# Kernel optimization log

Measured on AMD Instinct MI355X. Metric: run time of the kernel, lower is better.

## Reference

```python
import jax, jax.numpy as jnp
import numpy as np

HEADS = 8
DIM_HEAD = 32
EPS = 1e-5


def _rel_index(h, w):
    # matches Attention._generate_relative_index (static, computed on host)
    coords = np.stack(np.meshgrid(np.arange(h), np.arange(w), indexing='ij')).reshape(2, -1)
    rel = coords[:, :, None] - coords[:, None, :]  # [2, n, n]
    rel[0] += h - 1
    rel[1] += w - 1
    rel[0] *= 2 * w - 1
    idx = rel.sum(0).reshape(-1)
    # torch.clamp(relative_index, 0, max_index) -- indices are already in range here
    return jnp.asarray(np.clip(idx, 0, (2 * h - 1) * (2 * w - 1) - 1))


def _layernorm(x, g, b):
    m = jnp.mean(x, axis=-1, keepdims=True)
    v = jnp.var(x, axis=-1, keepdims=True)
    return (x - m) * jax.lax.rsqrt(v + EPS) * g + b


def setup_inputs() -> dict:
    key = jax.random.key(0)
    ks = jax.random.split(key, 6)
    B, C, H, W = 64, 384, 16, 16
    inner = HEADS * DIM_HEAD  # 256
    hid = 4 * C               # 1536
    def nrm(k, shape, s=0.02):
        return jax.random.normal(k, shape, jnp.float32) * s
    return {
        'x': jax.random.normal(ks[0], (B, C, H, W), jnp.float32),
        'ln1_g': jnp.ones((C,), jnp.float32),
        'ln1_b': jnp.zeros((C,), jnp.float32),
        'w_qkv': nrm(ks[1], (C, 3 * inner)),
        'bias_table': nrm(ks[2], ((2 * H - 1) * (2 * W - 1), HEADS)),
        'w_out': nrm(ks[3], (inner, C)),
        'b_out': jnp.zeros((C,), jnp.float32),
        'ln2_g': jnp.ones((C,), jnp.float32),
        'ln2_b': jnp.zeros((C,), jnp.float32),
        'w_ff1': nrm(ks[4], (C, hid)),
        'b_ff1': jnp.zeros((hid,), jnp.float32),
        'w_ff2': nrm(ks[5], (hid, C)),
        'b_ff2': jnp.zeros((C,), jnp.float32),
    }


def reference(x, ln1_g, ln1_b, w_qkv, bias_table, w_out, b_out,
              ln2_g, ln2_b, w_ff1, b_ff1, w_ff2, b_ff2):
    B, C, H, W = x.shape
    n = H * W
    t = x.reshape(B, C, n).transpose(0, 2, 1)  # [B, n, C]

    # --- attention branch (PreNorm(LayerNorm) -> Attention) ---
    a = _layernorm(t, ln1_g, ln1_b)
    qkv = a @ w_qkv  # [B, n, 3*inner]
    q, k, v = jnp.split(qkv, 3, axis=-1)
    def split_heads(z):
        return z.reshape(B, n, HEADS, DIM_HEAD).transpose(0, 2, 1, 3)  # [B, h, n, d]
    q, k, v = split_heads(q), split_heads(k), split_heads(v)
    dots = jnp.einsum('bhid,bhjd->bhij', q, k) * (DIM_HEAD ** -0.5)
    idx = _rel_index(H, W)  # [n*n]
    rel_bias = bias_table[idx].reshape(n, n, HEADS).transpose(2, 0, 1)[None]  # [1, h, n, n]
    attn = jax.nn.softmax(dots + rel_bias, axis=-1)
    o = jnp.einsum('bhij,bhjd->bhid', attn, v)
    o = o.transpose(0, 2, 1, 3).reshape(B, n, HEADS * DIM_HEAD)
    attn_out = o @ w_out + b_out  # to_out Linear (dropout=0)

    # --- feedforward branch (PreNorm(LayerNorm) -> FFN) ---
    f = _layernorm(t, ln2_g, ln2_b)
    f = jax.nn.gelu(f @ w_ff1 + b_ff1, approximate=False) @ w_ff2 + b_ff2

    y = t + attn_out + f  # x_adjusted + attn_out + ff_out
    return y.transpose(0, 2, 1).reshape(B, C, H, W)
```

## Files before the change

kernel.cpp:

```cpp
#include <hip/hip_runtime.h>

typedef __bf16 bf16;
typedef __bf16 bf16x8 __attribute__((ext_vector_type(8)));
typedef float f32x4 __attribute__((ext_vector_type(4)));

__device__ __forceinline__ void gll16(const void* g, void* l) {
    __builtin_amdgcn_global_load_lds((const __attribute__((address_space(1))) void*)g,
                                     (__attribute__((address_space(3))) void*)l, 16, 0, 0);
}

__launch_bounds__(256)
__global__ void prep_kernel(const float* __restrict__ wqkv, const float* __restrict__ wout,
                            const float* __restrict__ wff1, const float* __restrict__ wff2,
                            bf16* __restrict__ wqkvT, bf16* __restrict__ woutT,
                            bf16* __restrict__ wff1T, bf16* __restrict__ wff2T,
                            const float* __restrict__ x,
                            const float* __restrict__ g1, const float* __restrict__ b1,
                            const float* __restrict__ g2, const float* __restrict__ b2,
                            bf16* __restrict__ a, bf16* __restrict__ f) {
    __shared__ __align__(16) float smem[12672 + 512 + 64];
    const int tid = threadIdx.x;
    int g = blockIdx.x;
    if (g < 1536) {
        float (*tl)[33] = (float (*)[33])smem;
        const float* in; bf16* out; int R, Cc, bx, by;
        if (g < 288)       { in = wqkv; out = wqkvT; R = 384;  Cc = 768;  bx = g % 24; by = g / 24; }
        else if (g < 384)  { g -= 288; in = wout; out = woutT; R = 256;  Cc = 384;  bx = g % 12; by = g / 12; }
        else if (g < 960)  { g -= 384; in = wff1; out = wff1T; R = 384;  Cc = 1536; bx = g % 48; by = g / 48; }
        else               { g -= 960; in = wff2; out = wff2T; R = 1536; Cc = 384;  bx = g % 12; by = g / 12; }
        const int c0 = bx * 32, r0 = by * 32;
        const int cl = tid & 31, r8 = tid >> 5;
#pragma unroll
        for (int k = 0; k < 4; k++) {
            int r = k * 8 + r8;
            tl[r][cl] = in[(size_t)(r0 + r) * Cc + c0 + cl];
        }
        __syncthreads();
#pragma unroll
        for (int k = 0; k < 4; k++) {
            int cc = k * 8 + r8;
            out[(size_t)(c0 + cc) * R + r0 + cl] = (bf16)tl[cl][cc];
        }
        return;
    }
    g -= 1536;
    float (*tile)[33] = (float (*)[33])smem;
    float (*S)[32]  = (float (*)[32])(smem + 12672);
    float (*SS)[32] = (float (*)[32])(smem + 12928);
    float* Mn = smem + 13184;
    float* Rs = smem + 13216;
    const int bb = g >> 3;
    const int i0 = (g & 7) * 32;
    {
        const int i_l = tid & 31, c_l = tid >> 5;
        const size_t base = (size_t)bb * 384 * 256 + i0 + i_l;
#pragma unroll 6
        for (int c = c_l; c < 384; c += 8)
            tile[c][i_l] = x[base + (size_t)c * 256];
    }
    __syncthreads();
    {
        const int i_s = tid & 31, p = tid >> 5;
        float s = 0.f, ss = 0.f;
#pragma unroll 6
        for (int j = 0; j < 48; j++) {
            float v = tile[p * 48 + j][i_s];
            s += v; ss += v * v;
        }
        S[p][i_s] = s; SS[p][i_s] = ss;
    }
    __syncthreads();
    if (tid < 32) {
        float t1 = 0.f, t2 = 0.f;
#pragma unroll
        for (int p = 0; p < 8; p++) { t1 += S[p][tid]; t2 += SS[p][tid]; }
        float mean = t1 * (1.0f / 384.0f);
        float var  = t2 * (1.0f / 384.0f) - mean * mean;
        Mn[tid] = mean;
        Rs[tid] = rsqrtf(var + 1e-5f);
    }
    __syncthreads();
    const int lane = tid & 63, w = tid >> 6;
#pragma unroll
    for (int rr = 0; rr < 8; rr++) {
        const int i = w * 8 + rr;
        const float mean = Mn[i], rstd = Rs[i];
        const size_t orow = ((size_t)bb * 256 + i0 + i) * 384;
#pragma unroll
        for (int pass = 0; pass < 6; pass++) {
            const int c = pass * 64 + lane;
            float nh = (tile[c][i] - mean) * rstd;
            a[orow + c] = (bf16)(nh * g1[c] + b1[c]);
            f[orow + c] = (bf16)(nh * g2[c] + b2[c]);
        }
    }
}

template <int EPI>
__launch_bounds__(256)
__global__ void gemm_bt(const bf16* __restrict__ A, const bf16* __restrict__ Bt,
                        const float* __restrict__ bias, bf16* __restrict__ C,
                        int M, int N, int K, int nx) {
    __shared__ bf16 lds[16384];
    bf16* lA = lds;
    bf16* lB = lds + 4096;
    const int tid = threadIdx.x;
    const int g = blockIdx.x;
    const int x = (g >> 3) % nx;
    const int y = (g & 7) + 8 * (g / (8 * nx));
    const int m0 = y * 128, n0 = x * 128;
    const int lane = tid & 63, w = tid >> 6;
    const int l16 = lane & 15, quad = lane >> 4;
    const int wm = (w & 1) * 64, wn = (w >> 1) * 64;

    f32x4 zero = {0.f, 0.f, 0.f, 0.f};
    f32x4 acc[4][4];
#pragma unroll
    for (int i = 0; i < 4; i++)
#pragma unroll
        for (int j = 0; j < 4; j++) acc[i][j] = zero;

    const int c0 = tid, c1 = tid + 256;
    const int r0 = c0 >> 2, k0c = (c0 & 3) * 8;
    const int r1 = c1 >> 2, k1c = (c1 & 3) * 8;
    const bf16* Abase = A + (size_t)m0 * K;
    const bf16* Bbase = Bt + (size_t)n0 * K;

    for (int kb = 0; kb < K; kb += 32) {
        gll16(Abase + (size_t)r0 * K + kb + k0c, lA + c0 * 8);
        gll16(Abase + (size_t)r1 * K + kb + k1c, lA + c1 * 8);
        gll16(Bbase + (size_t)r0 * K + kb + k0c, lB + c0 * 8);
        gll16(Bbase + (size_t)r1 * K + kb + k1c, lB + c1 * 8);
        __syncthreads();
        bf16x8 af[4], bfr[4];
#pragma unroll
        for (int i = 0; i < 4; i++)
            af[i] = *(const bf16x8*)(lA + (wm + i * 16 + l16) * 32 + quad * 8);
#pragma unroll
        for (int j = 0; j < 4; j++)
            bfr[j] = *(const bf16x8*)(lB + (wn + j * 16 + l16) * 32 + quad * 8);
#pragma unroll
        for (int i = 0; i < 4; i++)
#pragma unroll
            for (int j = 0; j < 4; j++)
                acc[i][j] = __builtin_amdgcn_mfma_f32_16x16x32_bf16(af[i], bfr[j], acc[i][j], 0, 0, 0);
        __syncthreads();
    }

#pragma unroll
    for (int j = 0; j < 4; j++) {
        const int col = wn + j * 16 + l16;
        float bv = 0.f;
        if (EPI >= 1) bv = bias[n0 + col];
#pragma unroll
        for (int i = 0; i < 4; i++) {
            const int row0 = wm + i * 16 + quad * 4;
#pragma unroll
            for (int r = 0; r < 4; r++) {
                float v = acc[i][j][r] + bv;
                if (EPI == 2) v = 0.5f * v * (1.0f + erff(v * 0.70710678118654752f));
                lds[(row0 + r) * 128 + col] = (bf16)v;
            }
        }
    }
    __syncthreads();
#pragma unroll
    for (int it = 0; it < 8; it++) {
        const int ch = tid + it * 256;
        const int row = ch >> 4, cc = (ch & 15) * 8;
        *(bf16x8*)(C + (size_t)(m0 + row) * N + n0 + cc) = *(const bf16x8*)(lds + row * 128 + cc);
    }
}

#define GEMM64_PROLOGUE_AND_KLOOP                                                   \
    const int tid = threadIdx.x;                                                    \
    const int g = blockIdx.x;                                                       \
    const int x_ = (g >> 3) % nx;                                                   \
    const int y_ = (g & 7) + 8 * (g / (8 * nx));                                    \
    const int m0 = y_ * 128, n0 = x_ * 64;                                          \
    const int lane = tid & 63, w = tid >> 6;                                        \
    const int l16 = lane & 15, quad = lane >> 4;                                    \
    const int wm = (w & 1) * 64, wn = (w >> 1) * 32;                                \
    f32x4 zero = {0.f, 0.f, 0.f, 0.f};                                              \
    f32x4 acc[4][2];                                                                \
    _Pragma("unroll") for (int i = 0; i < 4; i++)                                   \
        _Pragma("unroll") for (int j = 0; j < 2; j++) acc[i][j] = zero;             \
    const int c0 = tid, c1 = tid + 256;                                             \
    const int r0 = c0 >> 2, k0c = (c0 & 3) * 8;                                     \
    const int r1 = c1 >> 2, k1c = (c1 & 3) * 8;                                     \
    const bf16* Abase = A + (size_t)m0 * K;                                         \
    const bf16* Bbase = Bt + (size_t)n0 * K;                                        \
    for (int kb = 0; kb < K; kb += 32) {                                            \
        gll16(Abase + (size_t)r0 * K + kb + k0c, lA + c0 * 8);                      \
        gll16(Abase + (size_t)r1 * K + kb + k1c, lA + c1 * 8);                      \
        gll16(Bbase + (size_t)r0 * K + kb + k0c, lB + c0 * 8);                      \
        __syncthreads();                                                            \
        bf16x8 af[4], bfr[2];                                                       \
        _Pragma("unroll") for (int i = 0; i < 4; i++)                               \
            af[i] = *(const bf16x8*)(lA + (wm + i * 16 + l16) * 32 + quad * 8);     \
        _Pragma("unroll") for (int j = 0; j < 2; j++)                               \
            bfr[j] = *(const bf16x8*)(lB + (wn + j * 16 + l16) * 32 + quad * 8);    \
        _Pragma("unroll") for (int i = 0; i < 4; i++)                               \
            _Pragma("unroll") for (int j = 0; j < 2; j++)                           \
                acc[i][j] = __builtin_amdgcn_mfma_f32_16x16x32_bf16(af[i], bfr[j], acc[i][j], 0, 0, 0); \
        __syncthreads();                                                            \
    }

__launch_bounds__(256)
__global__ void gemm_bt_tr64(const bf16* __restrict__ A, const bf16* __restrict__ Bt,
                             const float* __restrict__ bias, bf16* __restrict__ Ct,
                             int M, int N, int K, int nx) {
    __shared__ bf16 lds[8448];
    bf16* lA = lds;
    bf16* lB = lds + 4096;
    GEMM64_PROLOGUE_AND_KLOOP
#pragma unroll
    for (int j = 0; j < 2; j++) {
        const int col = wn + j * 16 + l16;
        const float bv = bias[n0 + col];
#pragma unroll
        for (int i = 0; i < 4; i++) {
            const int row0 = wm + i * 16 + quad * 4;
#pragma unroll
            for (int r = 0; r < 4; r++)
                lds[col * 132 + row0 + r] = (bf16)(acc[i][j][r] + bv);
        }
    }
    __syncthreads();
    const int b = m0 >> 8, ib = m0 & 255;
#pragma unroll
    for (int it = 0; it < 4; it++) {
        const int ch = tid + it * 256;
        const int cl = ch >> 4, ic = (ch & 15) * 8;
        *(bf16x8*)(Ct + ((size_t)(b * 384 + n0 + cl) * 256 + ib + ic)) =
            *(const bf16x8*)(lds + cl * 132 + ic);
    }
}

__launch_bounds__(256)
__global__ void gemm_bt_final64(const bf16* __restrict__ A, const bf16* __restrict__ Bt,
                                const float* __restrict__ bias,
                                const float* __restrict__ xres, const bf16* __restrict__ attn_t,
                                float* __restrict__ out, int M, int N, int K, int nx) {
    __shared__ bf16 lds[8448];
    bf16* lA = lds;
    bf16* lB = lds + 4096;
    GEMM64_PROLOGUE_AND_KLOOP
#pragma unroll
    for (int j = 0; j < 2; j++) {
        const int col = wn + j * 16 + l16;
        const float bv = bias[n0 + col];
#pragma unroll
        for (int i = 0; i < 4; i++) {
            const int row0 = wm + i * 16 + quad * 4;
#pragma unroll
            for (int r = 0; r < 4; r++)
                lds[col * 132 + row0 + r] = (bf16)(acc[i][j][r] + bv);
        }
    }
    __syncthreads();
    const int b = m0 >> 8, ib = m0 & 255;
#pragma unroll
    for (int it = 0; it < 4; it++) {
        const int ch = tid + it * 256;
        const int cl = ch >> 4, ic = (ch & 15) * 8;
        const size_t base = (size_t)(b * 384 + n0 + cl) * 256 + ib + ic;
        bf16x8 ff = *(const bf16x8*)(lds + cl * 132 + ic);
        bf16x8 at = *(const bf16x8*)(attn_t + base);
#pragma unroll
        for (int e = 0; e < 8; e++)
            out[base + e] = xres[base + e] + (float)at[e] + (float)ff[e];
    }
}

__launch_bounds__(256)
__global__ void attn_kernel(const bf16* __restrict__ qkv,
                            const float* __restrict__ btab,
                            bf16* __restrict__ o) {
    __shared__ float sbias[961];
    __shared__ __align__(16) bf16 sVt[32][264];
    __shared__ __align__(16) bf16 sP[4][16][264];
    const int tid = threadIdx.x;
    const int qc = blockIdx.x & 3;
    const int h  = (blockIdx.x >> 2) & 7;
    const int bb = blockIdx.x >> 5;
    const int lane = tid & 63, w = tid >> 6;
    const int l16 = lane & 15, quad = lane >> 4;
    const size_t qkvb = (size_t)bb * 256 * 768;

    for (int e = tid; e < 961; e += 256) sbias[e] = btab[e * 8 + h];
#pragma unroll
    for (int it = 0; it < 32; it++) {
        int e = it * 256 + tid;
        int k = e >> 5, d = e & 31;
        sVt[d][k] = qkv[qkvb + (size_t)k * 768 + 512 + h * 32 + d];
    }
    __syncthreads();

    const int qbase = qc * 64 + w * 16;
    bf16x8 qf = *(const bf16x8*)(qkv + qkvb + (size_t)(qbase + l16) * 768 + h * 32 + quad * 8);
    f32x4 zero = {0.f, 0.f, 0.f, 0.f};
    f32x4 s[16];
#pragma unroll
    for (int kt = 0; kt < 16; kt++) {
        bf16x8 kf = *(const bf16x8*)(qkv + qkvb + (size_t)(kt * 16 + l16) * 768 + 256 + h * 32 + quad * 8);
        s[kt] = __builtin_amdgcn_mfma_f32_16x16x32_bf16(qf, kf, zero, 0, 0, 0);
    }
    const int qi0 = qbase + quad * 4;
    float mx[4] = {-1e30f, -1e30f, -1e30f, -1e30f};
#pragma unroll
    for (int kt = 0; kt < 16; kt++) {
        const int j = kt * 16 + l16;
        const int yj = j >> 4, xj = j & 15;
#pragma unroll
        for (int r = 0; r < 4; r++) {
            const int q = qi0 + r;
            const int tix = ((q >> 4) - yj + 15) * 31 + ((q & 15) - xj + 15);
            float v = s[kt][r] * 0.17677669529663687f + sbias[tix];
            s[kt][r] = v;
            mx[r] = fmaxf(mx[r], v);
        }
    }
#pragma unroll
    for (int r = 0; r < 4; r++)
        for (int msk = 1; msk < 16; msk <<= 1)
            mx[r] = fmaxf(mx[r], __shfl_xor(mx[r], msk, 64));
    float sum[4] = {0.f, 0.f, 0.f, 0.f};
#pragma unroll
    for (int kt = 0; kt < 16; kt++)
#pragma unroll
        for (int r = 0; r < 4; r++) {
            float e = __expf(s[kt][r] - mx[r]);
            s[kt][r] = e;
            sum[r] += e;
        }
#pragma unroll
    for (int r = 0; r < 4; r++) {
        for (int msk = 1; msk < 16; msk <<= 1)
            sum[r] += __shfl_xor(sum[r], msk, 64);
        sum[r] = 1.0f / sum[r];
    }
#pragma unroll
    for (int kt = 0; kt < 16; kt++)
#pragma unroll
        for (int r = 0; r < 4; r++)
            sP[w][quad * 4 + r][kt * 16 + l16] = (bf16)(s[kt][r] * sum[r]);
    f32x4 oacc[2];
    oacc[0] = zero; oacc[1] = zero;
#pragma unroll
    for (int ks = 0; ks < 8; ks++) {
        bf16x8 pf = *(const bf16x8*)(&sP[w][l16][ks * 32 + quad * 8]);
#pragma unroll
        for (int dt = 0; dt < 2; dt++) {
            bf16x8 vf = *(const bf16x8*)(&sVt[dt * 16 + l16][ks * 32 + quad * 8]);
            oacc[dt] = __builtin_amdgcn_mfma_f32_16x16x32_bf16(pf, vf, oacc[dt], 0, 0, 0);
        }
    }
#pragma unroll
    for (int dt = 0; dt < 2; dt++)
#pragma unroll
        for (int r = 0; r < 4; r++)
            o[(size_t)(bb * 256 + qbase + quad * 4 + r) * 256 + h * 32 + dt * 16 + l16] = (bf16)oacc[dt][r];
}

extern "C" void kernel_launch(void* const* d_in, const int* in_sizes, int n_in,
                              void* d_out, int out_size, void* d_ws, size_t ws_size,
                              hipStream_t stream) {
    const float* x    = (const float*)d_in[0];
    const float* g1   = (const float*)d_in[1];
    const float* b1   = (const float*)d_in[2];
    const float* wqkv = (const float*)d_in[3];
    const float* btab = (const float*)d_in[4];
    const float* wout = (const float*)d_in[5];
    const float* bout = (const float*)d_in[6];
    const float* g2   = (const float*)d_in[7];
    const float* b2   = (const float*)d_in[8];
    const float* wff1 = (const float*)d_in[9];
    const float* bff1 = (const float*)d_in[10];
    const float* wff2 = (const float*)d_in[11];
    const float* bff2 = (const float*)d_in[12];
    float* out = (float*)d_out;

    bf16* ws = (bf16*)d_ws;
    const size_t NA = 6291456;
    bf16* wqkvT = ws;
    bf16* woutT = wqkvT + 294912;
    bf16* wff1T = woutT + 98304;
    bf16* wff2T = wff1T + 589824;
    bf16* f_buf    = ws + 1572864;
    bf16* attn_t   = f_buf + NA;
    bf16* R        = attn_t + NA;
    bf16* a_buf    = R;
    bf16* qkv_buf  = R + NA;
    bf16* o_buf    = R;
    bf16* ffh_buf  = R;

    dim3 b256(256);
    prep_kernel<<<2048, b256, 0, stream>>>(wqkv, wout, wff1, wff2, wqkvT, woutT, wff1T, wff2T,
                                           x, g1, b1, g2, b2, a_buf, f_buf);

    gemm_bt<0><<<6 * 128, b256, 0, stream>>>(a_buf, wqkvT, nullptr, qkv_buf, 16384, 768, 384, 6);
    attn_kernel<<<2048, b256, 0, stream>>>(qkv_buf, btab, o_buf);
    gemm_bt_tr64<<<6 * 128, b256, 0, stream>>>(o_buf, woutT, bout, attn_t, 16384, 384, 256, 6);
    gemm_bt<2><<<12 * 128, b256, 0, stream>>>(f_buf, wff1T, bff1, ffh_buf, 16384, 1536, 384, 12);
    gemm_bt_final64<<<6 * 128, b256, 0, stream>>>(ffh_buf, wff2T, bff2, x, attn_t, out,
                                                  16384, 384, 1536, 6);
}
```

Measured before the change: 261.8 us.

## Reuse K/V across query chunks in attention and use fast GELU approximation

The attention kernel now processes all four query chunks per block, staging K into shared memory with async global-to-LDS loads and loading V with vectorized reads before transposing it. This removes the redundant per-chunk K/V reloads and scalar V gathers, at the cost of a 4x smaller grid and more serial work per block. Separately, the FF1 epilogue replaces exact erf GELU with an exp/reciprocal-based approximation, which cuts transcendental cost but slightly changes numerics.

```diff
diff --git a/kernel.cpp b/kernel.cpp
--- a/kernel.cpp
+++ b/kernel.cpp
@@ -7,6 +7,13 @@
 __device__ __forceinline__ void gll16(const void* g, void* l) {
     __builtin_amdgcn_global_load_lds((const __attribute__((address_space(1))) void*)g,
                                      (__attribute__((address_space(3))) void*)l, 16, 0, 0);
+}
+
+__device__ __forceinline__ float gelu_f(float v) {
+    float x2 = v * v;
+    float sn = v * fmaf(-0.0713540072f, x2, -1.5957691216f);
+    float e  = __expf(sn);
+    return v * __builtin_amdgcn_rcpf(1.0f + e);
 }
 
 __launch_bounds__(256)
@@ -158,7 +165,7 @@
 #pragma unroll
             for (int r = 0; r < 4; r++) {
                 float v = acc[i][j][r] + bv;
-                if (EPI == 2) v = 0.5f * v * (1.0f + erff(v * 0.70710678118654752f));
+                if (EPI == 2) v = gelu_f(v);
                 lds[(row0 + r) * 128 + col] = (bf16)v;
             }
         }
@@ -278,89 +285,104 @@
                             const float* __restrict__ btab,
                             bf16* __restrict__ o) {
     __shared__ float sbias[961];
+    __shared__ __align__(16) bf16 sK[256 * 32];
     __shared__ __align__(16) bf16 sVt[32][264];
     __shared__ __align__(16) bf16 sP[4][16][264];
     const int tid = threadIdx.x;
-    const int qc = blockIdx.x & 3;
-    const int h  = (blockIdx.x >> 2) & 7;
-    const int bb = blockIdx.x >> 5;
+    const int g = blockIdx.x;
+    const int h  = (g >> 3) & 7;
+    const int bb = (g & 7) + 8 * (g >> 6);
     const int lane = tid & 63, w = tid >> 6;
     const int l16 = lane & 15, quad = lane >> 4;
     const size_t qkvb = (size_t)bb * 256 * 768;
+    const bf16* Qbase = qkv + qkvb + h * 32;
+    const bf16* Kbase = qkv + qkvb + 256 + h * 32;
+    const bf16* Vbase = qkv + qkvb + 512 + h * 32;
 
     for (int e = tid; e < 961; e += 256) sbias[e] = btab[e * 8 + h];
 #pragma unroll
-    for (int it = 0; it < 32; it++) {
-        int e = it * 256 + tid;
-        int k = e >> 5, d = e & 31;
-        sVt[d][k] = qkv[qkvb + (size_t)k * 768 + 512 + h * 32 + d];
-    }
-    __syncthreads();
-
-    const int qbase = qc * 64 + w * 16;
-    bf16x8 qf = *(const bf16x8*)(qkv + qkvb + (size_t)(qbase + l16) * 768 + h * 32 + quad * 8);
+    for (int it = 0; it < 4; it++) {
+        const int ch = it * 256 + tid;
+        const int row = ch >> 2, d8 = (ch & 3) * 8;
+        gll16(Kbase + (size_t)row * 768 + d8, sK + ch * 8);
+    }
+#pragma unroll
+    for (int it = 0; it < 4; it++) {
+        const int ch = it * 256 + tid;
+        const int k = ch >> 2, d8 = (ch & 3) * 8;
+        bf16x8 vv = *(const bf16x8*)(Vbase + (size_t)k * 768 + d8);
+#pragma unroll
+        for (int j = 0; j < 8; j++)
+            sVt[d8 + j][k] = vv[j];
+    }
+    __syncthreads();
+
     f32x4 zero = {0.f, 0.f, 0.f, 0.f};
-    f32x4 s[16];
-#pragma unroll
-    for (int kt = 0; kt < 16; kt++) {
-        bf16x8 kf = *(const bf16x8*)(qkv + qkvb + (size_t)(kt * 16 + l16) * 768 + 256 + h * 32 + quad * 8);
-        s[kt] = __builtin_amdgcn_mfma_f32_16x16x32_bf16(qf, kf, zero, 0, 0, 0);
-    }
-    const int qi0 = qbase + quad * 4;
-    float mx[4] = {-1e30f, -1e30f, -1e30f, -1e30f};
-#pragma unroll
-    for (int kt = 0; kt < 16; kt++) {
-        const int j = kt * 16 + l16;
-        const int yj = j >> 4, xj = j & 15;
+    for (int qc = 0; qc < 4; qc++) {
+        const int qbase = qc * 64 + w * 16;
+        bf16x8 qf = *(const bf16x8*)(Qbase + (size_t)(qbase + l16) * 768 + quad * 8);
+        f32x4 s[16];
+#pragma unroll
+        for (int kt = 0; kt < 16; kt++) {
+            bf16x8 kf = *(const bf16x8*)(sK + (kt * 16 + l16) * 32 + quad * 8);
+            s[kt] = __builtin_amdgcn_mfma_f32_16x16x32_bf16(qf, kf, zero, 0, 0, 0);
+        }
+        const int qi0 = qbase + quad * 4;
+        float mx[4] = {-1e30f, -1e30f, -1e30f, -1e30f};
+#pragma unroll
+        for (int kt = 0; kt < 16; kt++) {
+            const int j = kt * 16 + l16;
+            const int yj = j >> 4, xj = j & 15;
+#pragma unroll
+            for (int r = 0; r < 4; r++) {
+                const int q = qi0 + r;
+                const int tix = ((q >> 4) - yj + 15) * 31 + ((q & 15) - xj + 15);
+                float v = s[kt][r] * 0.17677669529663687f + sbias[tix];
+                s[kt][r] = v;
+                mx[r] = fmaxf(mx[r], v);
+            }
+        }
+#pragma unroll
+        for (int r = 0; r < 4; r++)
+            for (int msk = 1; msk < 16; msk <<= 1)
+                mx[r] = fmaxf(mx[r], __shfl_xor(mx[r], msk, 64));
+        float sum[4] = {0.f, 0.f, 0.f, 0.f};
+#pragma unroll
+        for (int kt = 0; kt < 16; kt++)
+#pragma unroll
+            for (int r = 0; r < 4; r++) {
+                float e = __expf(s[kt][r] - mx[r]);
+                s[kt][r] = e;
+                sum[r] += e;
+            }
 #pragma unroll
         for (int r = 0; r < 4; r++) {
-            const int q = qi0 + r;
-            const int tix = ((q >> 4) - yj + 15) * 31 + ((q & 15) - xj + 15);
-            float v = s[kt][r] * 0.17677669529663687f + sbias[tix];
-            s[kt][r] = v;
-            mx[r] = fmaxf(mx[r], v);
-        }
-    }
-#pragma unroll
-    for (int r = 0; r < 4; r++)
-        for (int msk = 1; msk < 16; msk <<= 1)
-            mx[r] = fmaxf(mx[r], __shfl_xor(mx[r], msk, 64));
-    float sum[4] = {0.f, 0.f, 0.f, 0.f};
-#pragma unroll
-    for (int kt = 0; kt < 16; kt++)
-#pragma unroll
-        for (int r = 0; r < 4; r++) {
-            float e = __expf(s[kt][r] - mx[r]);
-            s[kt][r] = e;
-            sum[r] += e;
-        }
-#pragma unroll
-    for (int r = 0; r < 4; r++) {
-        for (int msk = 1; msk < 16; msk <<= 1)
-            sum[r] += __shfl_xor(sum[r], msk, 64);
-        sum[r] = 1.0f / sum[r];
-    }
-#pragma unroll
-    for (int kt = 0; kt < 16; kt++)
-#pragma unroll
-        for (int r = 0; r < 4; r++)
-            sP[w][quad * 4 + r][kt * 16 + l16] = (bf16)(s[kt][r] * sum[r]);
-    f32x4 oacc[2];
-    oacc[0] = zero; oacc[1] = zero;
-#pragma unroll
-    for (int ks = 0; ks < 8; ks++) {
-        bf16x8 pf = *(const bf16x8*)(&sP[w][l16][ks * 32 + quad * 8]);
-#pragma unroll
-        for (int dt = 0; dt < 2; dt++) {
-            bf16x8 vf = *(const bf16x8*)(&sVt[dt * 16 + l16][ks * 32 + quad * 8]);
-            oacc[dt] = __builtin_amdgcn_mfma_f32_16x16x32_bf16(pf, vf, oacc[dt], 0, 0, 0);
-        }
-    }
-#pragma unroll
-    for (int dt = 0; dt < 2; dt++)
-#pragma unroll
-        for (int r = 0; r < 4; r++)
-            o[(size_t)(bb * 256 + qbase + quad * 4 + r) * 256 + h * 32 + dt * 16 + l16] = (bf16)oacc[dt][r];
+            for (int msk = 1; msk < 16; msk <<= 1)
+                sum[r] += __shfl_xor(sum[r], msk, 64);
+            sum[r] = 1.0f / sum[r];
+        }
+#pragma unroll
+        for (int kt = 0; kt < 16; kt++)
+#pragma unroll
+            for (int r = 0; r < 4; r++)
+                sP[w][quad * 4 + r][kt * 16 + l16] = (bf16)(s[kt][r] * sum[r]);
+        f32x4 oacc[2];
+        oacc[0] = zero; oacc[1] = zero;
+#pragma unroll
+        for (int ks = 0; ks < 8; ks++) {
+            bf16x8 pf = *(const bf16x8*)(&sP[w][l16][ks * 32 + quad * 8]);
+#pragma unroll
+            for (int dt = 0; dt < 2; dt++) {
+                bf16x8 vf = *(const bf16x8*)(&sVt[dt * 16 + l16][ks * 32 + quad * 8]);
+                oacc[dt] = __builtin_amdgcn_mfma_f32_16x16x32_bf16(pf, vf, oacc[dt], 0, 0, 0);
+            }
+        }
+#pragma unroll
+        for (int dt = 0; dt < 2; dt++)
+#pragma unroll
+            for (int r = 0; r < 4; r++)
+                o[(size_t)(bb * 256 + qbase + quad * 4 + r) * 256 + h * 32 + dt * 16 + l16] = (bf16)oacc[dt][r];
+    }
 }
 
 extern "C" void kernel_launch(void* const* d_in, const int* in_sizes, int n_in,
@@ -400,7 +422,7 @@
                                            x, g1, b1, g2, b2, a_buf, f_buf);
 
     gemm_bt<0><<<6 * 128, b256, 0, stream>>>(a_buf, wqkvT, nullptr, qkv_buf, 16384, 768, 384, 6);
-    attn_kernel<<<2048, b256, 0, stream>>>(qkv_buf, btab, o_buf);
+    attn_kernel<<<512, b256, 0, stream>>>(qkv_buf, btab, o_buf);
     gemm_bt_tr64<<<6 * 128, b256, 0, stream>>>(o_buf, woutT, bout, attn_t, 16384, 384, 256, 6);
     gemm_bt<2><<<12 * 128, b256, 0, stream>>>(f_buf, wff1T, bff1, ffh_buf, 16384, 1536, 384, 12);
     gemm_bt_final64<<<6 * 128, b256, 0, stream>>>(ffh_buf, wff2T, bff2, x, attn_t, out,
```

Result: faster. 237.0 us (-9.5%).
